# Optimization experiments

Measured on AMD Instinct MI355X. Metric: run time of the kernel, lower is better.

## Reference

```python
import jax, jax.numpy as jnp
import numpy as np

N_NODES = 50000
N_EDGES = 500000
D_MODEL = 128
D_INNER = 256
N_EXPERT = 64
TOP_K = 2
CAP_FACTOR = 2  # capacity factor for expert dispatch (fastmoe has no drop; factor 2 is ample for ~uniform gates)
BN_EPS = 1e-5


def setup_inputs() -> dict:
    key = jax.random.key(0)
    ks = jax.random.split(key, 12)
    d, h, E = D_MODEL, D_INNER, N_EXPERT
    return {
        "feats": jax.random.normal(ks[0], (N_NODES, d), jnp.float32),
        "edge_src": jax.random.randint(ks[1], (N_EDGES,), 0, N_NODES),
        "edge_dst": jax.random.randint(ks[2], (N_EDGES,), 0, N_NODES),
        "W_conv": jax.random.normal(ks[3], (d, d), jnp.float32) / np.sqrt(d),
        "b_conv": jnp.zeros((d,), jnp.float32),
        "gate_W": jax.random.normal(ks[4], (d, E), jnp.float32) / np.sqrt(d),
        "gate_b": jnp.zeros((E,), jnp.float32),
        "W1": jax.random.normal(ks[5], (E, d, h), jnp.float32) / np.sqrt(d),
        "b1": jnp.zeros((E, h), jnp.float32),
        "W2": jax.random.normal(ks[6], (E, h, d), jnp.float32) / np.sqrt(h),
        "b2": jnp.zeros((E, d), jnp.float32),
        "bn_gamma": jnp.ones((d,), jnp.float32),
        "bn_beta": jnp.zeros((d,), jnp.float32),
    }


def _gcn_conv(feats, edge_src, edge_dst, W_conv, b_conv):
    # symmetric-normalized sum aggregation over edge list
    n = feats.shape[0]
    ones = jnp.ones_like(edge_dst, dtype=feats.dtype)
    deg = jax.ops.segment_sum(ones, edge_dst, num_segments=n)
    deg = jnp.maximum(deg, 1.0)
    inv_sqrt = jax.lax.rsqrt(deg)
    norm = inv_sqrt[edge_src] * inv_sqrt[edge_dst]          # [Ed]
    msgs = feats[edge_src] * norm[:, None]                  # [Ed, d]
    agg = jax.ops.segment_sum(msgs, edge_dst, num_segments=n)
    return agg @ W_conv + b_conv


def _moe_ffn(x, gate_W, gate_b, W1, b1, W2, b2):
    # fastmoe NaiveGate: top-k of linear gate, softmax over the top-k scores
    T, d = x.shape
    E, h = W1.shape[0], W1.shape[2]
    scores = x @ gate_W + gate_b                            # [T, E]
    topv, topi = jax.lax.top_k(scores, TOP_K)               # [T, k]
    gw = jax.nn.softmax(topv, axis=-1)                      # [T, k]

    P = T * TOP_K
    eid = topi.reshape(P)                                   # expert id per (token, slot)
    x_rep = jnp.repeat(x, TOP_K, axis=0)                    # [P, d]

    onehot = jax.nn.one_hot(eid, E, dtype=jnp.int32)        # [P, E]
    pos = jnp.sum(jnp.cumsum(onehot, axis=0) * onehot, axis=-1) - 1  # rank within expert
    C = CAP_FACTOR * int(np.ceil(P / E))
    valid = pos < C
    slot = eid * C + jnp.where(valid, pos, 0)               # [P]

    buf = jnp.zeros((E * C, d), x.dtype).at[slot].add(
        jnp.where(valid[:, None], x_rep, 0.0))
    buf = buf.reshape(E, C, d)
    hact = jax.nn.gelu(jnp.einsum('ecd,edh->ech', buf, W1) + b1[:, None, :],
                       approximate=False)
    y = jnp.einsum('ech,ehd->ecd', hact, W2) + b2[:, None, :]
    y_pairs = y.reshape(E * C, d)[slot] * valid[:, None].astype(x.dtype)  # [P, d]
    y_pairs = y_pairs.reshape(T, TOP_K, d)
    return jnp.einsum('tk,tkd->td', gw, y_pairs)


def _batchnorm(x, gamma, beta):
    mean = jnp.mean(x, axis=0)
    var = jnp.mean(jnp.square(x - mean), axis=0)  # biased, as torch BN training
    return (x - mean) * jax.lax.rsqrt(var + BN_EPS) * gamma + beta


def reference(feats, edge_src, edge_dst, W_conv, b_conv, gate_W, gate_b,
              W1, b1, W2, b2, bn_gamma, bn_beta):
    new_feats = _gcn_conv(feats, edge_src, edge_dst, W_conv, b_conv)
    core = _moe_ffn(new_feats, gate_W, gate_b, W1, b1, W2, b2)
    # dropout p=0.0 -> identity; BN(inp + core_out)
    return _batchnorm(new_feats + core, bn_gamma, bn_beta)
```

## Files before the change

### kernel.cpp

```cpp
#include <hip/hip_runtime.h>
#include <math.h>

#define N_NODES 50000
#define N_EDGES 500000
#define D 128
#define H 256
#define NE 64
#define TOPK 2
#define NPAIR (N_NODES * TOPK)
#define CAP 3126
#define TILE_R 32
#define BQ 16
#define BN_NBLK 128
#define BN_ROWS ((N_NODES + BN_NBLK - 1) / BN_NBLK)

typedef __attribute__((ext_vector_type(8))) short s16x8;
typedef __attribute__((ext_vector_type(4))) float f32x4;

__device__ __forceinline__ unsigned short f2bf(float f) {
    unsigned u = __float_as_uint(f);
    unsigned r = (u + 0x7fffu + ((u >> 16) & 1u)) >> 16;
    return (unsigned short)r;
}
__device__ __forceinline__ float bf2f(unsigned short u) {
    return __uint_as_float(((unsigned)u) << 16);
}

#define DOT2(s, c, xx, ww) {                      \
    float p_ = (xx) * (ww);                       \
    float e1_ = fmaf((xx), (ww), -p_);            \
    float t_ = (s) + p_;                          \
    float z_ = t_ - (s);                          \
    float e2_ = ((s) - (t_ - z_)) + (p_ - z_);    \
    (s) = t_;                                     \
    (c) += e1_ + e2_; }

#define TSUM(s, c, pp) {                          \
    float p_ = (pp);                              \
    float t_ = (s) + p_;                          \
    float z_ = t_ - (s);                          \
    float e2_ = ((s) - (t_ - z_)) + (p_ - z_);    \
    (s) = t_;                                     \
    (c) += e2_; }

__global__ void k_deg(const int* __restrict__ dst, int* __restrict__ deg) {
    int i = blockIdx.x * blockDim.x + threadIdx.x;
    if (i < N_EDGES) atomicAdd(&deg[dst[i]], 1);
}

__global__ void k_invsqrt(const int* __restrict__ deg, float* __restrict__ invs) {
    int i = blockIdx.x * blockDim.x + threadIdx.x;
    if (i < N_NODES) {
        double d = (double)deg[i];
        if (d < 1.0) d = 1.0;
        invs[i] = (float)(1.0 / sqrt(d));
    }
}

__global__ __launch_bounds__(1024) void k_scan(const int* __restrict__ deg,
                                               int* __restrict__ rowptr) {
    __shared__ int sh[1024];
    int t = threadIdx.x;
    const int chunk = (N_NODES + 1023) / 1024;
    int lo = t * chunk;
    int hi = min(lo + chunk, N_NODES);
    int s = 0;
    for (int i = lo; i < hi; i++) s += deg[i];
    sh[t] = s;
    __syncthreads();
    for (int off = 1; off < 1024; off <<= 1) {
        int v = (t >= off) ? sh[t - off] : 0;
        __syncthreads();
        sh[t] += v;
        __syncthreads();
    }
    int run = (t == 0) ? 0 : sh[t - 1];
    for (int i = lo; i < hi; i++) { rowptr[i] = run; run += deg[i]; }
    if (t == 1023) rowptr[N_NODES] = run;
}

__global__ void k_scatter(const int* __restrict__ src, const int* __restrict__ dst,
                          const int* __restrict__ rowptr, int* __restrict__ cursor,
                          int* __restrict__ csr) {
    int e = blockIdx.x * blockDim.x + threadIdx.x;
    if (e >= N_EDGES) return;
    int d = dst[e];
    int pos = atomicAdd(&cursor[d], 1);
    csr[rowptr[d] + pos] = src[e];
}

__global__ __launch_bounds__(256) void k_gather(const float* __restrict__ feats,
                                                const int* __restrict__ rowptr,
                                                const int* __restrict__ csr,
                                                const float* __restrict__ invs,
                                                float* __restrict__ agg) {
    int node = blockIdx.x * 4 + (threadIdx.x >> 6);
    if (node >= N_NODES) return;
    int lane = threadIdx.x & 63;
    int beg = rowptr[node], end = rowptr[node + 1];
    float wd = invs[node];
    float sx = 0.f, cx = 0.f, sy = 0.f, cy = 0.f;
    for (int i = beg; i < end; i++) {
        int s = csr[i];
        float nrm = invs[s] * wd;
        float2 f = ((const float2*)(feats + (size_t)s * D))[lane];
        DOT2(sx, cx, nrm, f.x);
        DOT2(sy, cy, nrm, f.y);
    }
    ((float2*)(agg + (size_t)node * D))[lane] = make_float2(sx + cx, sy + cy);
}

__global__ __launch_bounds__(256) void k_conv(const float* __restrict__ agg,
                                              const float* __restrict__ W,
                                              const float* __restrict__ bias,
                                              float* __restrict__ out) {
    __shared__ float Wl[D * D];
    __shared__ float xl[TILE_R * D];
    int r0 = blockIdx.x * TILE_R;
    int rows = min(TILE_R, N_NODES - r0);
    for (int i = threadIdx.x; i < D * D / 4; i += 256)
        ((float4*)Wl)[i] = ((const float4*)W)[i];
    for (int i = threadIdx.x; i < rows * 32; i += 256) {
        int r = i >> 5, q = i & 31;
        ((float4*)(xl + r * D))[q] = ((const float4*)(agg + (size_t)(r0 + r) * D))[q];
    }
    __syncthreads();
    int c = threadIdx.x & 127;
    int half = threadIdx.x >> 7;
    float acc[16];
#pragma unroll
    for (int j = 0; j < 16; j++) acc[j] = 0.f;
    for (int k = 0; k < D; k++) {
        float w = Wl[k * D + c];
#pragma unroll
        for (int j = 0; j < 16; j++) acc[j] += xl[(half + j * 2) * D + k] * w;
    }
    float b = bias[c];
#pragma unroll
    for (int j = 0; j < 16; j++) {
        int r = half + j * 2;
        if (r < rows) out[(size_t)(r0 + r) * D + c] = acc[j] + b;
    }
}

__global__ __launch_bounds__(256, 4) void k_gate(const float* __restrict__ nf,
                                                 const float* __restrict__ gW,
                                                 const float* __restrict__ gb,
                                                 float* __restrict__ gwout,
                                                 int* __restrict__ topi,
                                                 int* __restrict__ rcnt,
                                                 int* __restrict__ redo) {
    __shared__ float Wl[D * NE];
    __shared__ float xsh[16 * D];
    for (int i = threadIdx.x; i < D * NE / 4; i += 256)
        ((float4*)Wl)[i] = ((const float4*)gW)[i];
    int t_base = blockIdx.x * 16;
    for (int i = threadIdx.x; i < 16 * 32; i += 256) {
        int r = i >> 5, q = i & 31;
        ((float4*)(xsh + r * D))[q] =
            ((const float4*)(nf + (size_t)(t_base + r) * D))[q];
    }
    __syncthreads();

    int wave = threadIdx.x >> 6;
    int lane = threadIdx.x & 63;
    int t0 = t_base + wave * 4;
    const float* xw = xsh + wave * 4 * D;

    float a0 = 0.f, a1 = 0.f, a2 = 0.f, a3 = 0.f;
#pragma unroll 4
    for (int k4 = 0; k4 < D; k4 += 4) {
        float x0[4], x1[4], x2[4], x3[4];
        *(float4*)x0 = *(const float4*)(xw + k4);
        *(float4*)x1 = *(const float4*)(xw + D + k4);
        *(float4*)x2 = *(const float4*)(xw + 2 * D + k4);
        *(float4*)x3 = *(const float4*)(xw + 3 * D + k4);
#pragma unroll
        for (int u = 0; u < 4; u++) {
            float w = Wl[(k4 + u) * NE + lane];
            a0 = fmaf(x0[u], w, a0);
            a1 = fmaf(x1[u], w, a1);
            a2 = fmaf(x2[u], w, a2);
            a3 = fmaf(x3[u], w, a3);
        }
    }
    float gbf = gb[lane];
    float af[4] = {a0 + gbf, a1 + gbf, a2 + gbf, a3 + gbf};

    const float TAU = 2e-4f;

#pragma unroll
    for (int j = 0; j < 4; j++) {
        float sf = (j == 0) ? af[0] : (j == 1) ? af[1] : (j == 2) ? af[2] : af[3];
        int t = t0 + j;

        float v1 = sf; int i1 = lane;
#pragma unroll
        for (int off = 32; off; off >>= 1) {
            float ov = __shfl_xor(v1, off);
            int   oi = __shfl_xor(i1, off);
            if (ov > v1 || (ov == v1 && oi < i1)) { v1 = ov; i1 = oi; }
        }
        float v2 = (lane == i1) ? -INFINITY : sf; int i2 = lane;
#pragma unroll
        for (int off = 32; off; off >>= 1) {
            float ov = __shfl_xor(v2, off);
            int   oi = __shfl_xor(i2, off);
            if (ov > v2 || (ov == v2 && oi < i2)) { v2 = ov; i2 = oi; }
        }
        float v3 = (lane == i1 || lane == i2) ? -INFINITY : sf;
#pragma unroll
        for (int off = 32; off; off >>= 1)
            v3 = fmaxf(v3, __shfl_xor(v3, off));

        if (lane == 0) {
            float dd = v2 - v1;
            float e2 = expf(dd);
            float g0 = 1.0f / (1.0f + e2);
            gwout[2 * t] = g0;
            gwout[2 * t + 1] = e2 * g0;
            topi[2 * t] = i1;
            topi[2 * t + 1] = i2;
            if ((v1 - v2 <= TAU) || (v2 - v3 <= TAU)) {
                int slot = atomicAdd(rcnt, 1);
                redo[slot] = t;
            }
        }
    }
}

__global__ __launch_bounds__(256) void k_gfix(const float* __restrict__ nf,
                                              const float* __restrict__ gW,
                                              const float* __restrict__ gb,
                                              const int* __restrict__ rcnt,
                                              const int* __restrict__ redo,
                                              float* __restrict__ gwout,
                                              int* __restrict__ topi) {
    int nredo = *rcnt;
    int lane = threadIdx.x & 63;
    int widx = blockIdx.x * 4 + (threadIdx.x >> 6);
    float gbf = gb[lane];
    for (int i = widx; i < nredo; i += gridDim.x * 4) {
        int t = redo[i];
        const float* xr = nf + (size_t)t * D;
        float s = 0.f, c = 0.f;
        for (int k = 0; k < D; k++)
            DOT2(s, c, xr[k], gW[k * NE + lane]);
        TSUM(s, c, gbf);
        float vv = s + c, rr = (s - vv) + c;

        float a1v = vv, a1r = rr; int i1 = lane;
#pragma unroll
        for (int off = 32; off; off >>= 1) {
            float ov = __shfl_xor(a1v, off);
            float orr = __shfl_xor(a1r, off);
            int   oi = __shfl_xor(i1, off);
            bool gt = (ov > a1v) || (ov == a1v && (orr > a1r || (orr == a1r && oi < i1)));
            if (gt) { a1v = ov; a1r = orr; i1 = oi; }
        }
        bool ex = (lane == i1);
        float a2v = ex ? -INFINITY : vv;
        float a2r = ex ? 0.f : rr;
        int i2 = lane;
#pragma unroll
        for (int off = 32; off; off >>= 1) {
            float ov = __shfl_xor(a2v, off);
            float orr = __shfl_xor(a2r, off);
            int   oi = __shfl_xor(i2, off);
            bool gt = (ov > a2v) || (ov == a2v && (orr > a2r || (orr == a2r && oi < i2)));
            if (gt) { a2v = ov; a2r = orr; i2 = oi; }
        }

        if (lane == 0) {
            float dd = (a2v - a1v) + (a2r - a1r);
            float e2 = expf(dd);
            float g0 = 1.0f / (1.0f + e2);
            gwout[2 * t] = g0;
            gwout[2 * t + 1] = e2 * g0;
            topi[2 * t] = i1;
            topi[2 * t + 1] = i2;
        }
    }
}

__global__ __launch_bounds__(1024) void k_disp(const int* __restrict__ topi,
                                               int* __restrict__ cnt,
                                               int* __restrict__ plist) {
    __shared__ int lcnt[NE];
    __shared__ int lbase[NE];
    int tid = threadIdx.x;
    if (tid < NE) lcnt[tid] = 0;
    __syncthreads();
    int p = blockIdx.x * 1024 + tid;
    int e = 0, lr = 0;
    bool act = (p < NPAIR);
    if (act) {
        e = topi[p];
        lr = atomicAdd(&lcnt[e], 1);
    }
    __syncthreads();
    if (tid < NE) {
        int n = lcnt[tid];
        lbase[tid] = n ? atomicAdd(&cnt[tid], n) : 0;
    }
    __syncthreads();
    if (act) {
        int slot = lbase[e] + lr;
        if (slot < CAP) plist[e * CAP + slot] = p;
    }
}

__global__ __launch_bounds__(256) void k_wconv(const float* __restrict__ W1,
                                               const float* __restrict__ W2,
                                               unsigned short* __restrict__ w1c,
                                               unsigned short* __restrict__ w2c) {
    int gid = blockIdx.x * 256 + threadIdx.x;
    const int NW1 = NE * 4 * 256 * 4;
    if (gid < NW1) {
        int lhi = gid & 3, h = (gid >> 2) & 255, ks = (gid >> 10) & 3, e = gid >> 12;
        int d0 = ks * 32 + lhi * 8;
        unsigned short v[8] __attribute__((aligned(16)));
#pragma unroll
        for (int j = 0; j < 8; j++)
            v[j] = f2bf(W1[((size_t)e * D + d0 + j) * H + h]);
        *(int4*)(w1c + (size_t)gid * 8) = *(int4*)v;
    } else {
        int g = gid - NW1;
        int lhi = g & 3, d = (g >> 2) & 127, ks = (g >> 9) & 7, e = g >> 12;
        int h0 = ks * 32 + lhi * 8;
        unsigned short v[8] __attribute__((aligned(16)));
#pragma unroll
        for (int j = 0; j < 8; j++)
            v[j] = f2bf(W2[((size_t)e * H + h0 + j) * D + d]);
        *(int4*)(w2c + (size_t)g * 8) = *(int4*)v;
    }
}

__global__ __launch_bounds__(512, 4) void k_moe(const float* __restrict__ nf,
                                                const int* __restrict__ cnt,
                                                const int* __restrict__ plist,
                                                const unsigned short* __restrict__ w1c,
                                                const float* __restrict__ b1,
                                                const unsigned short* __restrict__ w2c,
                                                const float* __restrict__ b2,
                                                const float* __restrict__ gwbuf,
                                                unsigned short* __restrict__ ybuf) {
    __shared__ __align__(16) char smem[32768];
    const int XA = 0, HL = 8192, YB = 24576;
    int e = blockIdx.x & 63;
    int q = blockIdx.x >> 6;
    int n = min(cnt[e], CAP);
    int ntile = (n + TILE_R - 1) / TILE_R;
    if (q >= ntile) return;
    int tid = threadIdx.x;

    int wv = tid >> 6, lane = tid & 63;
    int lhi = lane >> 4, llo = lane & 15;
    int sr = tid >> 4, ss = tid & 15;
    f32x4 zero = {0.f, 0.f, 0.f, 0.f};

    s16x8 w1f[4][2];
#pragma unroll
    for (int ks = 0; ks < 4; ks++)
#pragma unroll
        for (int nt = 0; nt < 2; nt++) {
            int h = wv * 32 + nt * 16 + llo;
            w1f[ks][nt] = *(const s16x8*)(w1c +
                ((size_t)e * 4096 + (ks * 256 + h) * 4 + lhi) * 8);
        }
    s16x8 w2f[8];
    {
        int d = wv * 16 + llo;
#pragma unroll
        for (int ks = 0; ks < 8; ks++)
            w2f[ks] = *(const s16x8*)(w2c +
                ((size_t)e * 4096 + (ks * 128 + d) * 4 + lhi) * 8);
    }

    float vals[8];
    auto loadt = [&](int rt2, float* v) {
        bool ok = false;
        if (rt2 < ntile) {
            int rows2 = min(TILE_R, n - rt2 * TILE_R);
            if (sr < rows2) {
                int p = plist[e * CAP + rt2 * TILE_R + sr];
                const float4* xr = (const float4*)(nf + (size_t)(p >> 1) * D + ss * 8);
                *(float4*)(v + 0) = xr[0];
                *(float4*)(v + 4) = xr[1];
                ok = true;
            }
        }
        if (!ok) {
#pragma unroll
            for (int k = 0; k < 8; k++) v[k] = 0.f;
        }
    };
    loadt(q, vals);

    for (int rt = q; rt < ntile; rt += BQ) {
        int r0 = rt * TILE_R;
        int rows = min(TILE_R, n - r0);
        __syncthreads();

        {
            unsigned short hb[8] __attribute__((aligned(16)));
#pragma unroll
            for (int k = 0; k < 8; k++) hb[k] = f2bf(vals[k]);
            *(int4*)(smem + XA + sr * 256 + ((ss * 16) ^ ((sr & 7) << 4))) = *(int4*)hb;
        }
        __syncthreads();

        loadt(rt + BQ, vals);

        f32x4 acc1[2][2];
#pragma unroll
        for (int mt = 0; mt < 2; mt++)
#pragma unroll
            for (int nt = 0; nt < 2; nt++) acc1[mt][nt] = zero;
#pragma unroll
        for (int ks = 0; ks < 4; ks++) {
            int kb = ks * 64 + lhi * 16;
            s16x8 a0 = *(const s16x8*)(smem + XA + llo * 256        + (kb ^ ((llo & 7) << 4)));
            s16x8 a1 = *(const s16x8*)(smem + XA + (llo + 16) * 256 + (kb ^ ((llo & 7) << 4)));
#pragma unroll
            for (int nt = 0; nt < 2; nt++) {
                acc1[0][nt] = __builtin_amdgcn_mfma_f32_16x16x32_bf16(a0, w1f[ks][nt], acc1[0][nt], 0, 0, 0);
                acc1[1][nt] = __builtin_amdgcn_mfma_f32_16x16x32_bf16(a1, w1f[ks][nt], acc1[1][nt], 0, 0, 0);
            }
        }

#pragma unroll
        for (int mt = 0; mt < 2; mt++)
#pragma unroll
            for (int nt = 0; nt < 2; nt++)
#pragma unroll
                for (int r = 0; r < 4; r++) {
                    int m = mt * 16 + lhi * 4 + r;
                    int hc = wv * 32 + nt * 16 + llo;
                    float hv = acc1[mt][nt][r] + b1[e * H + hc];
                    float g = 0.5f * hv * (1.0f + erff(hv * 0.70710678118654752f));
                    *(unsigned short*)(smem + HL + m * 512 + ((hc * 2) ^ ((m & 7) << 4))) = f2bf(g);
                }
        __syncthreads();

        f32x4 acc2[2];
        acc2[0] = zero; acc2[1] = zero;
#pragma unroll
        for (int ks = 0; ks < 8; ks++) {
            int kb = ks * 64 + lhi * 16;
            s16x8 a0 = *(const s16x8*)(smem + HL + llo * 512        + (kb ^ ((llo & 7) << 4)));
            s16x8 a1 = *(const s16x8*)(smem + HL + (llo + 16) * 512 + (kb ^ ((llo & 7) << 4)));
            acc2[0] = __builtin_amdgcn_mfma_f32_16x16x32_bf16(a0, w2f[ks], acc2[0], 0, 0, 0);
            acc2[1] = __builtin_amdgcn_mfma_f32_16x16x32_bf16(a1, w2f[ks], acc2[1], 0, 0, 0);
        }

        {
            int d = wv * 16 + llo;
            float bb = b2[e * D + d];
#pragma unroll
            for (int mt = 0; mt < 2; mt++)
#pragma unroll
                for (int r = 0; r < 4; r++) {
                    int m = mt * 16 + lhi * 4 + r;
                    *(unsigned short*)(smem + YB + m * 256 + ((d * 2) ^ ((m & 7) << 4))) =
                        f2bf(acc2[mt][r] + bb);
                }
        }
        __syncthreads();

        if (sr < rows) {
            int p = plist[e * CAP + r0 + sr];
            float gw = gwbuf[p];
            unsigned short yv[8] __attribute__((aligned(16)));
            *(int4*)yv = *(const int4*)(smem + YB + sr * 256 + ((ss * 16) ^ ((sr & 7) << 4)));
#pragma unroll
            for (int k = 0; k < 8; k++) yv[k] = f2bf(gw * bf2f(yv[k]));
            *(int4*)(ybuf + (size_t)p * D + ss * 8) = *(int4*)yv;
        }
    }
}

__global__ __launch_bounds__(256) void k_bnpart(const float* __restrict__ nf,
                                                const unsigned short* __restrict__ ybuf,
                                                double* __restrict__ part) {
    int blk = blockIdx.x;
    int col = threadIdx.x & 127;
    int half = threadIdx.x >> 7;
    int r0 = blk * BN_ROWS;
    int r1 = min(r0 + BN_ROWS, N_NODES);
    double s = 0.0, ss = 0.0;
    for (int r = r0 + half; r < r1; r += 2) {
        float v32 = nf[(size_t)r * D + col]
                  + bf2f(ybuf[(size_t)(2 * r) * D + col])
                  + bf2f(ybuf[(size_t)(2 * r + 1) * D + col]);
        double v = (double)v32;
        s += v; ss += v * v;
    }
    __shared__ double sh[2][256];
    sh[0][threadIdx.x] = s; sh[1][threadIdx.x] = ss;
    __syncthreads();
    if (threadIdx.x < 128) {
        part[(size_t)blk * 256 + col]       = sh[0][col] + sh[0][col + 128];
        part[(size_t)blk * 256 + 128 + col] = sh[1][col] + sh[1][col + 128];
    }
}

__global__ void k_bnstats(const double* __restrict__ part,
                          const float* __restrict__ gamma,
                          float* __restrict__ stats) {
    int col = threadIdx.x;
    double s = 0.0, ss = 0.0;
    for (int b = 0; b < BN_NBLK; b++) {
        s  += part[(size_t)b * 256 + col];
        ss += part[(size_t)b * 256 + 128 + col];
    }
    double mean = s / (double)N_NODES;
    double var = ss / (double)N_NODES - mean * mean;
    stats[col] = (float)mean;
    stats[128 + col] = gamma[col] * (float)(1.0 / sqrt(var + 1e-5));
}

__global__ __launch_bounds__(256) void k_bnapply(const unsigned short* __restrict__ ybuf,
                                                 const float* __restrict__ stats,
                                                 const float* __restrict__ beta,
                                                 float* __restrict__ out) {
    int i = blockIdx.x * blockDim.x + threadIdx.x;
    if (i >= N_NODES * (D / 4)) return;
    int t = i >> 5;
    int q = i & 31;
    int c0 = q * 4;
    float4 v  = ((float4*)out)[i];
    short4 y0v = *(const short4*)(ybuf + (size_t)(2 * t) * D + c0);
    short4 y1v = *(const short4*)(ybuf + (size_t)(2 * t + 1) * D + c0);
    float4 r;
    r.x = (v.x + bf2f((unsigned short)y0v.x) + bf2f((unsigned short)y1v.x) - stats[c0 + 0]) * stats[128 + c0 + 0] + beta[c0 + 0];
    r.y = (v.y + bf2f((unsigned short)y0v.y) + bf2f((unsigned short)y1v.y) - stats[c0 + 1]) * stats[128 + c0 + 1] + beta[c0 + 1];
    r.z = (v.z + bf2f((unsigned short)y0v.z) + bf2f((unsigned short)y1v.z) - stats[c0 + 2]) * stats[128 + c0 + 2] + beta[c0 + 2];
    r.w = (v.w + bf2f((unsigned short)y0v.w) + bf2f((unsigned short)y1v.w) - stats[c0 + 3]) * stats[128 + c0 + 3] + beta[c0 + 3];
    ((float4*)out)[i] = r;
}

extern "C" void kernel_launch(void* const* d_in, const int* in_sizes, int n_in,
                              void* d_out, int out_size, void* d_ws, size_t ws_size,
                              hipStream_t stream) {
    const float* feats   = (const float*)d_in[0];
    const int*   esrc    = (const int*)d_in[1];
    const int*   edst    = (const int*)d_in[2];
    const float* W_conv  = (const float*)d_in[3];
    const float* b_conv  = (const float*)d_in[4];
    const float* gate_W  = (const float*)d_in[5];
    const float* gate_b  = (const float*)d_in[6];
    const float* W1      = (const float*)d_in[7];
    const float* b1      = (const float*)d_in[8];
    const float* W2      = (const float*)d_in[9];
    const float* b2      = (const float*)d_in[10];
    const float* bn_g    = (const float*)d_in[11];
    const float* bn_b    = (const float*)d_in[12];
    float* out = (float*)d_out;

    char* ws = (char*)d_ws;
    size_t off = 0;
    auto rup = [](size_t x) { return (x + 255) & ~(size_t)255; };
    int*    deg    = (int*)   (ws + off); off += rup((size_t)N_NODES * 4);
    int*    cursor = (int*)   (ws + off); off += rup((size_t)N_NODES * 4);
    int*    cnt    = (int*)   (ws + off); off += 256;
    int*    rcnt   = (int*)   (ws + off); off += 256;
    size_t zero_bytes = off;
    float*  invs   = (float*) (ws + off); off += rup((size_t)N_NODES * 4);
    int*    rowptr = (int*)   (ws + off); off += rup((size_t)(N_NODES + 1) * 4);
    int*    csr    = (int*)   (ws + off); off += rup((size_t)N_EDGES * 4);
    float*  gwbuf  = (float*) (ws + off); off += rup((size_t)NPAIR * 4);
    int*    topi   = (int*)   (ws + off); off += rup((size_t)NPAIR * 4);
    int*    redo   = (int*)   (ws + off); off += rup((size_t)N_NODES * 4);
    int*    plist  = (int*)   (ws + off); off += rup((size_t)NE * CAP * 4);
    double* part   = (double*)(ws + off); off += rup((size_t)BN_NBLK * 256 * 8);
    float*  stats  = (float*) (ws + off); off += 1024;
    unsigned short* w1c = (unsigned short*)(ws + off); off += rup((size_t)NE * D * H * 2);
    unsigned short* w2c = (unsigned short*)(ws + off); off += rup((size_t)NE * D * H * 2);
    unsigned short* ybuf = (unsigned short*)(ws + off); off += rup((size_t)NPAIR * D * 2);
    float*  agg    = (float*)ybuf;
    (void)ws_size; (void)in_sizes; (void)n_in; (void)out_size;

    hipMemsetAsync(d_ws, 0, zero_bytes, stream);

    k_wconv<<<2 * NE * 4 * 256 * 4 / 256, 256, 0, stream>>>(W1, W2, w1c, w2c);
    k_deg<<<(N_EDGES + 255) / 256, 256, 0, stream>>>(edst, deg);
    k_invsqrt<<<(N_NODES + 255) / 256, 256, 0, stream>>>(deg, invs);
    k_scan<<<1, 1024, 0, stream>>>(deg, rowptr);
    k_scatter<<<(N_EDGES + 255) / 256, 256, 0, stream>>>(esrc, edst, rowptr, cursor, csr);
    k_gather<<<(N_NODES + 3) / 4, 256, 0, stream>>>(feats, rowptr, csr, invs, agg);
    k_conv<<<(N_NODES + TILE_R - 1) / TILE_R, 256, 0, stream>>>(agg, W_conv, b_conv, out);
    k_gate<<<N_NODES / 16, 256, 0, stream>>>(out, gate_W, gate_b, gwbuf, topi, rcnt, redo);
    k_gfix<<<128, 256, 0, stream>>>(out, gate_W, gate_b, rcnt, redo, gwbuf, topi);
    k_disp<<<(NPAIR + 1023) / 1024, 1024, 0, stream>>>(topi, cnt, plist);
    k_moe<<<NE * BQ, 512, 0, stream>>>(out, cnt, plist, w1c, b1, w2c, b2, gwbuf, ybuf);
    k_bnpart<<<BN_NBLK, 256, 0, stream>>>(out, ybuf, part);
    k_bnstats<<<1, 128, 0, stream>>>(part, bn_g, stats);
    k_bnapply<<<(N_NODES * (D / 4) + 255) / 256, 256, 0, stream>>>(ybuf, stats, bn_b, out);
}
```

Baseline: 492.0 us.

## Unroll gather with Kahan sums, fast GELU polynomial, drop redundant barrier

The neighbor gather loop is unrolled by four so more independent row loads are in flight, and the TwoSum/TwoProd compensation is replaced by cheaper Kahan summation. The libm erff in the expert GELU is replaced by an Abramowitz-Stegun polynomial using a fast exp. A __syncthreads at the top of the expert tile loop is removed on the assumption that the later barriers already order the shared-memory accesses. This trades a little accuracy and some sync safety for fewer instructions and less latency.

```diff
diff --git a/kernel.cpp b/kernel.cpp
--- a/kernel.cpp
+++ b/kernel.cpp
@@ -26,6 +26,18 @@
     return __uint_as_float(((unsigned)u) << 16);
 }
 
+__device__ __forceinline__ float gelu_f(float x) {
+    float u = 0.70710678118654752f * x;
+    float au = fabsf(u);
+    float t = 1.0f / fmaf(0.3275911f, au, 1.0f);
+    float poly = t * fmaf(t, fmaf(t, fmaf(t, fmaf(t, 1.061405429f, -1.453152027f),
+                      1.421413741f), -0.284496736f), 0.254829592f);
+    float e = __expf(-u * u);
+    float erfa = 1.0f - poly * e;
+    float erfu = copysignf(erfa, u);
+    return 0.5f * x * (1.0f + erfu);
+}
+
 #define DOT2(s, c, xx, ww) {                      \
     float p_ = (xx) * (ww);                       \
     float e1_ = fmaf((xx), (ww), -p_);            \
@@ -42,6 +54,12 @@
     float e2_ = ((s) - (t_ - z_)) + (p_ - z_);    \
     (s) = t_;                                     \
     (c) += e2_; }
+
+#define KAH(s, c, pp) {                           \
+    float y_ = (pp) - (c);                        \
+    float t_ = (s) + y_;                          \
+    (c) = (t_ - (s)) - y_;                        \
+    (s) = t_; }
 
 __global__ void k_deg(const int* __restrict__ dst, int* __restrict__ deg) {
     int i = blockIdx.x * blockDim.x + threadIdx.x;
@@ -100,14 +118,28 @@
     int beg = rowptr[node], end = rowptr[node + 1];
     float wd = invs[node];
     float sx = 0.f, cx = 0.f, sy = 0.f, cy = 0.f;
-    for (int i = beg; i < end; i++) {
+    int i = beg;
+    for (; i + 4 <= end; i += 4) {
+        int s0 = csr[i], s1 = csr[i + 1], s2 = csr[i + 2], s3 = csr[i + 3];
+        float n0 = invs[s0] * wd, n1 = invs[s1] * wd;
+        float n2 = invs[s2] * wd, n3 = invs[s3] * wd;
+        float2 f0 = ((const float2*)(feats + (size_t)s0 * D))[lane];
+        float2 f1 = ((const float2*)(feats + (size_t)s1 * D))[lane];
+        float2 f2 = ((const float2*)(feats + (size_t)s2 * D))[lane];
+        float2 f3 = ((const float2*)(feats + (size_t)s3 * D))[lane];
+        KAH(sx, cx, n0 * f0.x); KAH(sy, cy, n0 * f0.y);
+        KAH(sx, cx, n1 * f1.x); KAH(sy, cy, n1 * f1.y);
+        KAH(sx, cx, n2 * f2.x); KAH(sy, cy, n2 * f2.y);
+        KAH(sx, cx, n3 * f3.x); KAH(sy, cy, n3 * f3.y);
+    }
+    for (; i < end; i++) {
         int s = csr[i];
         float nrm = invs[s] * wd;
         float2 f = ((const float2*)(feats + (size_t)s * D))[lane];
-        DOT2(sx, cx, nrm, f.x);
-        DOT2(sy, cy, nrm, f.y);
-    }
-    ((float2*)(agg + (size_t)node * D))[lane] = make_float2(sx + cx, sy + cy);
+        KAH(sx, cx, nrm * f.x);
+        KAH(sy, cy, nrm * f.y);
+    }
+    ((float2*)(agg + (size_t)node * D))[lane] = make_float2(sx, sy);
 }
 
 __global__ __launch_bounds__(256) void k_conv(const float* __restrict__ agg,
@@ -400,7 +432,6 @@
     for (int rt = q; rt < ntile; rt += BQ) {
         int r0 = rt * TILE_R;
         int rows = min(TILE_R, n - r0);
-        __syncthreads();
 
         {
             unsigned short hb[8] __attribute__((aligned(16)));
@@ -438,8 +469,8 @@
                     int m = mt * 16 + lhi * 4 + r;
                     int hc = wv * 32 + nt * 16 + llo;
                     float hv = acc1[mt][nt][r] + b1[e * H + hc];
-                    float g = 0.5f * hv * (1.0f + erff(hv * 0.70710678118654752f));
-                    *(unsigned short*)(smem + HL + m * 512 + ((hc * 2) ^ ((m & 7) << 4))) = f2bf(g);
+                    *(unsigned short*)(smem + HL + m * 512 + ((hc * 2) ^ ((m & 7) << 4))) =
+                        f2bf(gelu_f(hv));
                 }
         __syncthreads();
 
```

Result: faster. 461.2 us (-6.2%).
